# Performance work log

Measured on AMD Instinct MI355X. Metric: run time of the kernel, lower is better.

## Reference

```python
import jax, jax.numpy as jnp
import numpy as np

DM, NEXPERTS, SETS, ESIZE = 1024, 32, 4, 32
B, S = 2, 8192


def setup_inputs() -> dict:
    key = jax.random.key(0)
    ks = jax.random.split(key, 7)
    sc = 0.02
    return {
        "x": jax.random.normal(ks[0], (B, S, DM), jnp.float32),
        "Wc": jax.random.normal(ks[1], (DM, NEXPERTS, SETS), jnp.float32) * sc,
        "bc": jax.random.normal(ks[2], (NEXPERTS, SETS), jnp.float32) * sc,
        "W1": jax.random.normal(ks[3], (NEXPERTS, SETS, DM, ESIZE), jnp.float32) * sc,
        "b1": jax.random.normal(ks[4], (NEXPERTS, SETS, ESIZE), jnp.float32) * sc,
        "W2": jax.random.normal(ks[5], (NEXPERTS, SETS, DM, ESIZE), jnp.float32) * sc,
        "b2": jax.random.normal(ks[6], (NEXPERTS, SETS, DM), jnp.float32) * sc,
    }


def reference(x, Wc, bc, W1, b1, W2, b2):
    b, s, d = x.shape
    g = Wc.shape[1]          # nexperts (= tokens per group)
    # group tokens: [..., (n g), d] -> [..., n, g, d]
    grouped = x.reshape(b, s // g, g, d)
    # controller logits: [b, n, t, e, s]
    logits = jnp.einsum('bntd,des->bntes', grouped, Wc) + bc
    # tie-breaker varying along the token axis (dim -3)
    tie = jnp.linspace(0.0, 1e-6, g, dtype=x.dtype).reshape(-1, 1, 1)
    logits = logits + tie
    # hard one-hot permutation: argmax over tokens per (expert, set)
    perm = (logits == jnp.max(logits, axis=-3, keepdims=True)).astype(x.dtype)
    # dispatch: [b, n, e, s, d]
    permuted = jnp.einsum('bntd,bntes->bnesd', grouped, perm)
    # per-(expert,set) MLP
    inner = jax.nn.relu(jnp.einsum('bnesd,esdf->bnesf', permuted, W1) + b1)
    result_permuted = jnp.einsum('bnesf,esdf->bnesd', inner, W2) + b2
    # combine back to tokens: [b, n, t, d]
    result = jnp.einsum('bnesd,bntes->bntd', result_permuted, perm)
    return result.reshape(b, s, d)
```

## Files before the change

### kernel.cpp

```cpp
#include <hip/hip_runtime.h>
#include <hip/hip_bf16.h>

#define DM   1024
#define NES  128
#define GT   32
#define NGRP 512
#define FSZ  32

typedef float f32x4 __attribute__((ext_vector_type(4)));
typedef short s16x8 __attribute__((ext_vector_type(8)));

#define GL2LDS(gp, lp) __builtin_amdgcn_global_load_lds(                      \
    (const __attribute__((address_space(1))) void*)(gp),                     \
    (__attribute__((address_space(3))) void*)(lp), 16, 0, 0)

__device__ inline unsigned short f2bf(float f) {
  union { float f; unsigned int u; } x; x.f = f;
  unsigned int r = x.u + 0x7fffu + ((x.u >> 16) & 1u);
  return (unsigned short)(r >> 16);
}
__device__ inline float bf2f(unsigned short h) {
  union { unsigned int u; float f; } x; x.u = ((unsigned int)h) << 16;
  return x.f;
}

__global__ __launch_bounds__(256, 2) void kA(const float* __restrict__ x,
                                             const float* __restrict__ Wc,
                                             const float* __restrict__ bc,
                                             unsigned int* __restrict__ sel,
                                             unsigned short* __restrict__ xb) {
  __shared__ float smem[10240];
  float* const wcsA = smem;
  float* const wcsB = smem + 4096;
  float* const xsA  = smem + 8192;
  float* const xsB  = smem + 9216;
  float* const lg   = smem;
  const int g   = blockIdx.x;
  const int tid = threadIdx.x;
  const int l   = tid & 63, w = tid >> 6;
  const int es0 = (tid & 31) * 4;
  const int t0  = (tid >> 5) * 4;
  const float* xg = x + (size_t)g * GT * DM;

  float acc[16], part[16];
#pragma unroll
  for (int i = 0; i < 16; ++i) acc[i] = 0.f;

  auto STAGE = [&](int c, float* wdst, float* xdst) {
    const int d0 = c * 32;
#pragma unroll
    for (int kk = 0; kk < 4; ++kk) {
      int e4 = w * 1024 + kk * 256 + l * 4;
      GL2LDS(Wc + (size_t)(d0 + (e4 >> 7)) * NES + (e4 & 127),
             wdst + w * 1024 + kk * 256);
    }
    int ex = w * 256 + l * 4;
    GL2LDS(xg + (size_t)(ex >> 5) * DM + d0 + (ex & 31), xdst + w * 256);
  };

  STAGE(0, wcsA, xsA);
  asm volatile("s_waitcnt vmcnt(0)" ::: "memory");
  __syncthreads();

  for (int c = 0; c < 32; ++c) {
    const int b = c & 1;
    const float* wp = b ? wcsB : wcsA;
    const float* xp = b ? xsB : xsA;
    if (c < 31) STAGE(c + 1, b ? wcsA : wcsB, b ? xsA : xsB);

    {
      int idx = tid * 4;
      float4 a4 = *(const float4*)&xp[idx];
      short4 v;
      v.x = (short)f2bf(a4.x); v.y = (short)f2bf(a4.y);
      v.z = (short)f2bf(a4.z); v.w = (short)f2bf(a4.w);
      *(short4*)&xb[((size_t)g * GT + (idx >> 5)) * DM + c * 32 + (idx & 31)] = v;
    }

    if ((c & 1) == 0) {
#pragma unroll
      for (int i = 0; i < 16; ++i) part[i] = 0.f;
    }
#pragma unroll 2
    for (int dd = 0; dd < 32; dd += 4) {
      float4 w0 = *(const float4*)&wp[(dd + 0) * NES + es0];
      float4 w1 = *(const float4*)&wp[(dd + 1) * NES + es0];
      float4 w2 = *(const float4*)&wp[(dd + 2) * NES + es0];
      float4 w3 = *(const float4*)&wp[(dd + 3) * NES + es0];
      float4 xv0 = *(const float4*)&xp[(t0 + 0) * 32 + dd];
      float4 xv1 = *(const float4*)&xp[(t0 + 1) * 32 + dd];
      float4 xv2 = *(const float4*)&xp[(t0 + 2) * 32 + dd];
      float4 xv3 = *(const float4*)&xp[(t0 + 3) * 32 + dd];
#define KSTEP(i, XV)                                                       \
      part[i*4+0] = fmaf(XV.x, w0.x, part[i*4+0]);                         \
      part[i*4+1] = fmaf(XV.x, w0.y, part[i*4+1]);                         \
      part[i*4+2] = fmaf(XV.x, w0.z, part[i*4+2]);                         \
      part[i*4+3] = fmaf(XV.x, w0.w, part[i*4+3]);                         \
      part[i*4+0] = fmaf(XV.y, w1.x, part[i*4+0]);                         \
      part[i*4+1] = fmaf(XV.y, w1.y, part[i*4+1]);                         \
      part[i*4+2] = fmaf(XV.y, w1.z, part[i*4+2]);                         \
      part[i*4+3] = fmaf(XV.y, w1.w, part[i*4+3]);                         \
      part[i*4+0] = fmaf(XV.z, w2.x, part[i*4+0]);                         \
      part[i*4+1] = fmaf(XV.z, w2.y, part[i*4+1]);                         \
      part[i*4+2] = fmaf(XV.z, w2.z, part[i*4+2]);                         \
      part[i*4+3] = fmaf(XV.z, w2.w, part[i*4+3]);                         \
      part[i*4+0] = fmaf(XV.w, w3.x, part[i*4+0]);                         \
      part[i*4+1] = fmaf(XV.w, w3.y, part[i*4+1]);                         \
      part[i*4+2] = fmaf(XV.w, w3.z, part[i*4+2]);                         \
      part[i*4+3] = fmaf(XV.w, w3.w, part[i*4+3]);
      KSTEP(0, xv0) KSTEP(1, xv1) KSTEP(2, xv2) KSTEP(3, xv3)
#undef KSTEP
    }
    if (c & 1) {
#pragma unroll
      for (int i = 0; i < 16; ++i) acc[i] += part[i];
    }
    asm volatile("s_waitcnt vmcnt(0)" ::: "memory");
    __syncthreads();
  }

#pragma unroll
  for (int i = 0; i < 4; ++i) {
    int t = t0 + i;
    float tie = (float)((double)t * (1e-6 / 31.0));
#pragma unroll
    for (int j = 0; j < 4; ++j) {
      int es = es0 + j;
      lg[t * NES + es] = (acc[i * 4 + j] + bc[es]) + tie;
    }
  }
  __syncthreads();
  if (tid < NES) {
    float m = -INFINITY;
    for (int t = 0; t < GT; ++t) m = fmaxf(m, lg[t * NES + tid]);
    unsigned int msk = 0u;
    for (int t = 0; t < GT; ++t) if (lg[t * NES + tid] == m) msk |= (1u << t);
    sel[(size_t)g * NES + tid] = msk;
  }
}

__global__ __launch_bounds__(256) void kW(const float* __restrict__ W1,
                                          const float* __restrict__ W2,
                                          unsigned short* __restrict__ W1f,
                                          unsigned short* __restrict__ W2f) {
  const int bid = blockIdx.x;
  if (bid < 2048) {
    int idx = bid * 256 + threadIdx.x;
    int l = idx & 63, nh = (idx >> 6) & 1, kt = (idx >> 7) & 31, es = idx >> 12;
    const float* src = W1 + ((size_t)es * DM + kt * 32 + (l >> 4) * 8) * FSZ
                          + nh * 16 + (l & 15);
    s16x8 v;
#pragma unroll
    for (int i = 0; i < 8; ++i) v[i] = (short)f2bf(src[(size_t)i * FSZ]);
    *(s16x8*)(W1f + (size_t)idx * 8) = v;
  } else {
    int idx = (bid - 2048) * 256 + threadIdx.x;
    int l = idx & 63, dt = (idx >> 6) & 63, es = idx >> 12;
    const float* src = W2 + ((size_t)es * DM + dt * 16 + (l & 15)) * FSZ + (l >> 4) * 8;
    float4 a = *(const float4*)src;
    float4 b = *(const float4*)(src + 4);
    s16x8 v;
    v[0] = (short)f2bf(a.x); v[1] = (short)f2bf(a.y);
    v[2] = (short)f2bf(a.z); v[3] = (short)f2bf(a.w);
    v[4] = (short)f2bf(b.x); v[5] = (short)f2bf(b.y);
    v[6] = (short)f2bf(b.z); v[7] = (short)f2bf(b.w);
    *(s16x8*)(W2f + (size_t)idx * 8) = v;
  }
}

__global__ __launch_bounds__(256, 2) void kBm(const unsigned short* __restrict__ xb,
                                              const unsigned short* __restrict__ W1f,
                                              const float* __restrict__ b1,
                                              const unsigned int* __restrict__ sel,
                                              unsigned short* __restrict__ innerb) {
  __shared__ unsigned short As[128 * 128];
  __shared__ int tokL[128];
  __shared__ unsigned int mulL[128];
  const int bid = blockIdx.x;
  const int es = bid >> 2, g0 = (bid & 3) * 128;
  const int tid = threadIdx.x;
  const int l = tid & 63, w = tid >> 6;
  const int r15 = l & 15, q = l >> 4;
  const int mw = w * 32;

  if (tid < 128) {
    unsigned int m = sel[(size_t)(g0 + tid) * NES + es];
    tokL[tid] = (g0 + tid) * GT + (__ffs(m) - 1);
    mulL[tid] = (m & (m - 1)) ? m : 0u;
  }

  const int r = tid >> 1, p = tid & 1;
  const int swz = (r & 7) << 4;
  const unsigned int dbase = (unsigned int)r * 256 + (unsigned int)p * 128;

  f32x4 acc[2][2];
#pragma unroll
  for (int i = 0; i < 2; ++i)
#pragma unroll
    for (int j = 0; j < 2; ++j) acc[i][j] = (f32x4){0.f, 0.f, 0.f, 0.f};

  for (int c = 0; c < 8; ++c) {
    __syncthreads();
    unsigned int mm = mulL[r];
    if (!mm) {
      const unsigned short* src = xb + (size_t)tokL[r] * DM + c * 128 + p * 64;
#pragma unroll
      for (int j = 0; j < 8; ++j) {
        s16x8 v = *(const s16x8*)(src + j * 8);
        *(s16x8*)((char*)As + ((dbase + j * 16) ^ swz)) = v;
      }
    } else {
      size_t grow = (size_t)(g0 + r) * GT;
#pragma unroll
      for (int j = 0; j < 8; ++j) {
        float av[8] = {0.f, 0.f, 0.f, 0.f, 0.f, 0.f, 0.f, 0.f};
        unsigned int m2 = mm;
        while (m2) {
          int tt = __ffs(m2) - 1; m2 &= m2 - 1;
          s16x8 v = *(const s16x8*)(xb + (grow + tt) * DM + c * 128 + p * 64 + j * 8);
#pragma unroll
          for (int k = 0; k < 8; ++k) av[k] += bf2f((unsigned short)v[k]);
        }
        s16x8 o;
#pragma unroll
        for (int k = 0; k < 8; ++k) o[k] = (short)f2bf(av[k]);
        *(s16x8*)((char*)As + ((dbase + j * 16) ^ swz)) = o;
      }
    }
    __syncthreads();

#pragma unroll
    for (int s = 0; s < 4; ++s) {
      const int ks = c * 4 + s;
      const unsigned short* bp = W1f + ((size_t)es * 32 + ks) * 1024 + l * 8;
      s16x8 bf0 = *(const s16x8*)bp;
      s16x8 bf1 = *(const s16x8*)(bp + 512);
      const int row0 = mw + r15, row1 = mw + 16 + r15;
      s16x8 a0 = *(const s16x8*)((char*)As +
                   (((unsigned)row0 * 256 + s * 64 + q * 16) ^ ((row0 & 7) << 4)));
      s16x8 a1 = *(const s16x8*)((char*)As +
                   (((unsigned)row1 * 256 + s * 64 + q * 16) ^ ((row1 & 7) << 4)));
      acc[0][0] = __builtin_amdgcn_mfma_f32_16x16x32_bf16(a0, bf0, acc[0][0], 0, 0, 0);
      acc[0][1] = __builtin_amdgcn_mfma_f32_16x16x32_bf16(a0, bf1, acc[0][1], 0, 0, 0);
      acc[1][0] = __builtin_amdgcn_mfma_f32_16x16x32_bf16(a1, bf0, acc[1][0], 0, 0, 0);
      acc[1][1] = __builtin_amdgcn_mfma_f32_16x16x32_bf16(a1, bf1, acc[1][1], 0, 0, 0);
    }
  }

  float bia0 = b1[es * FSZ + r15];
  float bia1 = b1[es * FSZ + 16 + r15];
#pragma unroll
  for (int i = 0; i < 2; ++i)
#pragma unroll
    for (int rr = 0; rr < 4; ++rr) {
      int g = g0 + mw + i * 16 + q * 4 + rr;
      unsigned short* op = innerb + ((size_t)es * NGRP + g) * FSZ;
      op[r15]      = f2bf(fmaxf(acc[i][0][rr] + bia0, 0.f));
      op[16 + r15] = f2bf(fmaxf(acc[i][1][rr] + bia1, 0.f));
    }
}

__global__ __launch_bounds__(256) void kC1(const unsigned short* __restrict__ innerb,
                                           const unsigned short* __restrict__ W2f,
                                           const float* __restrict__ b2,
                                           unsigned short* __restrict__ Rb,
                                           int es0, int Ec) {
  const int bid = blockIdx.x;
  const int esl = bid >> 5;
  const int es  = es0 + esl;
  const int mt  = (bid >> 3) & 3;
  const int nt  = bid & 7;
  const int tid = threadIdx.x;
  const int l = tid & 63, w = tid >> 6;
  const int r15 = l & 15, q = l >> 4;
  const int g0 = mt * 128 + (w >> 1) * 64;
  const int n0 = nt * 128 + (w & 1) * 64;

  const unsigned short* Ab = innerb + ((size_t)es * NGRP + g0 + r15) * FSZ + q * 8;
  const unsigned short* Bb = W2f + (((size_t)es * 64 + (n0 >> 4)) * 64 + l) * 8;
  s16x8 a[4], b[4];
#pragma unroll
  for (int i = 0; i < 4; ++i) a[i] = *(const s16x8*)(Ab + (size_t)i * 16 * FSZ);
#pragma unroll
  for (int j = 0; j < 4; ++j) b[j] = *(const s16x8*)(Bb + (size_t)j * 64 * 8);

  const f32x4 z = {0.f, 0.f, 0.f, 0.f};
  f32x4 acc[4][4];
#pragma unroll
  for (int i = 0; i < 4; ++i)
#pragma unroll
    for (int j = 0; j < 4; ++j)
      acc[i][j] = __builtin_amdgcn_mfma_f32_16x16x32_bf16(a[i], b[j], z, 0, 0, 0);

#pragma unroll
  for (int j = 0; j < 4; ++j) {
    const int col = n0 + j * 16 + r15;
    const float b2v = b2[(size_t)es * DM + col];
#pragma unroll
    for (int i = 0; i < 4; ++i) {
#pragma unroll
      for (int r = 0; r < 4; ++r) {
        const int g = g0 + i * 16 + q * 4 + r;
        Rb[((size_t)g * Ec + esl) * DM + col] = f2bf(acc[i][j][r] + b2v);
      }
    }
  }
}

__global__ __launch_bounds__(256) void kC2(const unsigned short* __restrict__ Rb,
                                           const unsigned int* __restrict__ sel,
                                           float* __restrict__ out,
                                           int es0, int Ec, int direct) {
  __shared__ unsigned int cnt[32];
  __shared__ unsigned char list[32][128];
  const int bid = blockIdx.x;
  const int g = bid >> 2, dq = bid & 3;
  const int tid = threadIdx.x;
  if (tid < 32) cnt[tid] = 0;
  __syncthreads();
  if (tid < Ec) {
    unsigned int m = sel[(size_t)g * NES + es0 + tid];
    while (m) { int t = __ffs(m) - 1; m &= m - 1;
      unsigned int p = atomicAdd(&cnt[t], 1u);
      list[t][p] = (unsigned char)tid; }
  }
  __syncthreads();
  const int t = tid >> 3, part = tid & 7;
  const int d0 = dq * 256 + part * 32;
  const int n = (int)cnt[t];
  const unsigned short* base = Rb + (size_t)g * Ec * DM + d0;

  float acc[32];
#pragma unroll
  for (int i = 0; i < 32; ++i) acc[i] = 0.f;

  s16x8 cur[4];
  if (n) {
    const unsigned short* r = base + (size_t)list[t][0] * DM;
#pragma unroll
    for (int v = 0; v < 4; ++v) cur[v] = *(const s16x8*)(r + v * 8);
  }
  for (int e = 0; e < n; ++e) {
    s16x8 nxt[4];
    const bool more = (e + 1 < n);
    if (more) {
      const unsigned short* r = base + (size_t)list[t][e + 1] * DM;
#pragma unroll
      for (int v = 0; v < 4; ++v) nxt[v] = *(const s16x8*)(r + v * 8);
    }
#pragma unroll
    for (int v = 0; v < 4; ++v)
#pragma unroll
      for (int k = 0; k < 8; ++k)
        acc[v * 8 + k] += bf2f((unsigned short)cur[v][k]);
    if (more) {
#pragma unroll
      for (int v = 0; v < 4; ++v) cur[v] = nxt[v];
    }
  }

  float* op = out + ((size_t)g * GT + t) * DM + d0;
  if (direct) {
#pragma unroll
    for (int v = 0; v < 8; ++v)
      *(float4*)&op[v * 4] =
          make_float4(acc[v * 4], acc[v * 4 + 1], acc[v * 4 + 2], acc[v * 4 + 3]);
  } else {
#pragma unroll
    for (int v = 0; v < 8; ++v) {
      float4 o = *(float4*)&op[v * 4];
      o.x += acc[v * 4]; o.y += acc[v * 4 + 1];
      o.z += acc[v * 4 + 2]; o.w += acc[v * 4 + 3];
      *(float4*)&op[v * 4] = o;
    }
  }
}

extern "C" void kernel_launch(void* const* d_in, const int* in_sizes, int n_in,
                              void* d_out, int out_size, void* d_ws, size_t ws_size,
                              hipStream_t stream) {
  const float* x  = (const float*)d_in[0];
  const float* Wc = (const float*)d_in[1];
  const float* bc = (const float*)d_in[2];
  const float* W1 = (const float*)d_in[3];
  const float* b1 = (const float*)d_in[4];
  const float* W2 = (const float*)d_in[5];
  const float* b2 = (const float*)d_in[6];
  float* out = (float*)d_out;

  unsigned int* sel = (unsigned int*)d_ws;
  unsigned short* innerb = (unsigned short*)((char*)d_ws + (1u << 20));
  unsigned short* W2f = (unsigned short*)((char*)d_ws + (6u << 20));
  unsigned short* W1f = (unsigned short*)((char*)d_ws + (15u << 20));
  unsigned short* xb  = (unsigned short*)((char*)d_ws + (24u << 20));
  unsigned short* Rb  = (unsigned short*)((char*)d_ws + (15u << 20));

  int Ec = 128;
  while (Ec > 1 && (15u << 20) + (size_t)NGRP * Ec * DM * 2 > ws_size) Ec >>= 1;
  const int NC = NES / Ec;

  if (NC > 1)
    hipMemsetAsync(d_out, 0, (size_t)out_size * sizeof(float), stream);
  kA<<<NGRP, 256, 0, stream>>>(x, Wc, bc, sel, xb);
  kW<<<4096, 256, 0, stream>>>(W1, W2, W1f, W2f);
  kBm<<<NGRP, 256, 0, stream>>>(xb, W1f, b1, sel, innerb);
  for (int c = 0; c < NC; ++c) {
    kC1<<<Ec * 32, 256, 0, stream>>>(innerb, W2f, b2, Rb, c * Ec, Ec);
    kC2<<<NGRP * 4, 256, 0, stream>>>(Rb, sel, out, c * Ec, Ec, NC == 1);
  }
}
```

Measured before the change: 214.3 us.

## Read Wc directly from global/L2 and stage larger x chunks in LDS

The controller-logit kernel no longer stages Wc through LDS. Each thread now reads its Wc float4 columns straight from global memory, relying on L2/L1 caching since every block shares Wc. Only x is double-buffered in LDS, in 128-wide chunks across 8 iterations instead of 32, which cuts barrier count and LDS footprint. The cost is more global load latency in the inner FMA loop, and partial sums are now flushed every 64 d-elements.

```diff
diff --git a/kernel.cpp b/kernel.cpp
--- a/kernel.cpp
+++ b/kernel.cpp
@@ -29,89 +29,88 @@
                                              const float* __restrict__ bc,
                                              unsigned int* __restrict__ sel,
                                              unsigned short* __restrict__ xb) {
-  __shared__ float smem[10240];
-  float* const wcsA = smem;
-  float* const wcsB = smem + 4096;
-  float* const xsA  = smem + 8192;
-  float* const xsB  = smem + 9216;
-  float* const lg   = smem;
+  __shared__ float smem[8192];
+  float* const xsA = smem;
+  float* const xsB = smem + 4096;
+  float* const lg  = smem;
   const int g   = blockIdx.x;
   const int tid = threadIdx.x;
   const int l   = tid & 63, w = tid >> 6;
   const int es0 = (tid & 31) * 4;
   const int t0  = (tid >> 5) * 4;
   const float* xg = x + (size_t)g * GT * DM;
+  const float* wbase = Wc + es0;
 
   float acc[16], part[16];
 #pragma unroll
   for (int i = 0; i < 16; ++i) acc[i] = 0.f;
 
-  auto STAGE = [&](int c, float* wdst, float* xdst) {
-    const int d0 = c * 32;
+  auto STAGE = [&](int c, float* dst) {
+    const int d0 = c * 128;
 #pragma unroll
     for (int kk = 0; kk < 4; ++kk) {
-      int e4 = w * 1024 + kk * 256 + l * 4;
-      GL2LDS(Wc + (size_t)(d0 + (e4 >> 7)) * NES + (e4 & 127),
-             wdst + w * 1024 + kk * 256);
-    }
-    int ex = w * 256 + l * 4;
-    GL2LDS(xg + (size_t)(ex >> 5) * DM + d0 + (ex & 31), xdst + w * 256);
+      const int inst = w * 4 + kk;
+      GL2LDS(xg + (size_t)(inst * 2 + (l >> 5)) * DM + d0 + (l & 31) * 4,
+             dst + inst * 256);
+    }
   };
 
-  STAGE(0, wcsA, xsA);
+  STAGE(0, xsA);
   asm volatile("s_waitcnt vmcnt(0)" ::: "memory");
   __syncthreads();
 
-  for (int c = 0; c < 32; ++c) {
-    const int b = c & 1;
-    const float* wp = b ? wcsB : wcsA;
-    const float* xp = b ? xsB : xsA;
-    if (c < 31) STAGE(c + 1, b ? wcsA : wcsB, b ? xsA : xsB);
-
-    {
-      int idx = tid * 4;
+  for (int c = 0; c < 8; ++c) {
+    const int d0 = c * 128;
+    const float* xp = (c & 1) ? xsB : xsA;
+    if (c < 7) STAGE(c + 1, (c & 1) ? xsA : xsB);
+
+#pragma unroll
+    for (int j = 0; j < 4; ++j) {
+      int idx = j * 1024 + tid * 4;
+      int t = idx >> 7, col = idx & 127;
       float4 a4 = *(const float4*)&xp[idx];
       short4 v;
       v.x = (short)f2bf(a4.x); v.y = (short)f2bf(a4.y);
       v.z = (short)f2bf(a4.z); v.w = (short)f2bf(a4.w);
-      *(short4*)&xb[((size_t)g * GT + (idx >> 5)) * DM + c * 32 + (idx & 31)] = v;
-    }
-
-    if ((c & 1) == 0) {
+      *(short4*)&xb[((size_t)g * GT + t) * DM + d0 + col] = v;
+    }
+
+#pragma unroll
+    for (int h = 0; h < 2; ++h) {
 #pragma unroll
       for (int i = 0; i < 16; ++i) part[i] = 0.f;
-    }
-#pragma unroll 2
-    for (int dd = 0; dd < 32; dd += 4) {
-      float4 w0 = *(const float4*)&wp[(dd + 0) * NES + es0];
-      float4 w1 = *(const float4*)&wp[(dd + 1) * NES + es0];
-      float4 w2 = *(const float4*)&wp[(dd + 2) * NES + es0];
-      float4 w3 = *(const float4*)&wp[(dd + 3) * NES + es0];
-      float4 xv0 = *(const float4*)&xp[(t0 + 0) * 32 + dd];
-      float4 xv1 = *(const float4*)&xp[(t0 + 1) * 32 + dd];
-      float4 xv2 = *(const float4*)&xp[(t0 + 2) * 32 + dd];
-      float4 xv3 = *(const float4*)&xp[(t0 + 3) * 32 + dd];
+#pragma unroll 4
+      for (int s = 0; s < 16; ++s) {
+        const int dd = h * 64 + s * 4;
+        const size_t wrow = (size_t)(d0 + dd) * NES;
+        float4 w0 = *(const float4*)&wbase[wrow];
+        float4 w1 = *(const float4*)&wbase[wrow + 128];
+        float4 w2 = *(const float4*)&wbase[wrow + 256];
+        float4 w3 = *(const float4*)&wbase[wrow + 384];
+        float4 xv0 = *(const float4*)&xp[(t0 + 0) * 128 + dd];
+        float4 xv1 = *(const float4*)&xp[(t0 + 1) * 128 + dd];
+        float4 xv2 = *(const float4*)&xp[(t0 + 2) * 128 + dd];
+        float4 xv3 = *(const float4*)&xp[(t0 + 3) * 128 + dd];
 #define KSTEP(i, XV)                                                       \
-      part[i*4+0] = fmaf(XV.x, w0.x, part[i*4+0]);                         \
-      part[i*4+1] = fmaf(XV.x, w0.y, part[i*4+1]);                         \
-      part[i*4+2] = fmaf(XV.x, w0.z, part[i*4+2]);                         \
-      part[i*4+3] = fmaf(XV.x, w0.w, part[i*4+3]);                         \
-      part[i*4+0] = fmaf(XV.y, w1.x, part[i*4+0]);                         \
-      part[i*4+1] = fmaf(XV.y, w1.y, part[i*4+1]);                         \
-      part[i*4+2] = fmaf(XV.y, w1.z, part[i*4+2]);                         \
-      part[i*4+3] = fmaf(XV.y, w1.w, part[i*4+3]);                         \
-      part[i*4+0] = fmaf(XV.z, w2.x, part[i*4+0]);                         \
-      part[i*4+1] = fmaf(XV.z, w2.y, part[i*4+1]);                         \
-      part[i*4+2] = fmaf(XV.z, w2.z, part[i*4+2]);                         \
-      part[i*4+3] = fmaf(XV.z, w2.w, part[i*4+3]);                         \
-      part[i*4+0] = fmaf(XV.w, w3.x, part[i*4+0]);                         \
-      part[i*4+1] = fmaf(XV.w, w3.y, part[i*4+1]);                         \
-      part[i*4+2] = fmaf(XV.w, w3.z, part[i*4+2]);                         \
-      part[i*4+3] = fmaf(XV.w, w3.w, part[i*4+3]);
-      KSTEP(0, xv0) KSTEP(1, xv1) KSTEP(2, xv2) KSTEP(3, xv3)
+        part[i*4+0] = fmaf(XV.x, w0.x, part[i*4+0]);                       \
+        part[i*4+1] = fmaf(XV.x, w0.y, part[i*4+1]);                       \
+        part[i*4+2] = fmaf(XV.x, w0.z, part[i*4+2]);                       \
+        part[i*4+3] = fmaf(XV.x, w0.w, part[i*4+3]);                       \
+        part[i*4+0] = fmaf(XV.y, w1.x, part[i*4+0]);                       \
+        part[i*4+1] = fmaf(XV.y, w1.y, part[i*4+1]);                       \
+        part[i*4+2] = fmaf(XV.y, w1.z, part[i*4+2]);                       \
+        part[i*4+3] = fmaf(XV.y, w1.w, part[i*4+3]);                       \
+        part[i*4+0] = fmaf(XV.z, w2.x, part[i*4+0]);                       \
+        part[i*4+1] = fmaf(XV.z, w2.y, part[i*4+1]);                       \
+        part[i*4+2] = fmaf(XV.z, w2.z, part[i*4+2]);                       \
+        part[i*4+3] = fmaf(XV.z, w2.w, part[i*4+3]);                       \
+        part[i*4+0] = fmaf(XV.w, w3.x, part[i*4+0]);                       \
+        part[i*4+1] = fmaf(XV.w, w3.y, part[i*4+1]);                       \
+        part[i*4+2] = fmaf(XV.w, w3.z, part[i*4+2]);                       \
+        part[i*4+3] = fmaf(XV.w, w3.w, part[i*4+3]);
+        KSTEP(0, xv0) KSTEP(1, xv1) KSTEP(2, xv2) KSTEP(3, xv3)
 #undef KSTEP
-    }
-    if (c & 1) {
+      }
 #pragma unroll
       for (int i = 0; i < 16; ++i) acc[i] += part[i];
     }
```

Measured after the change: 289.9 us. 1.35x slower.
